# Performance work log

Hardware: AMD Instinct MI355X
Metric: run time of the kernel (lower is better)

The kernel has to match this reference:

```python
import jax, jax.numpy as jnp
import numpy as np

B, S, D = 2, 2048, 1024
H, KS = 16, 64

def setup_inputs() -> dict:
    key = jax.random.key(0)
    k1, k2, k3, k4, k5 = jax.random.split(key, 5)
    return {
        "x": jax.random.normal(k1, (B, S, D), dtype=jnp.float32),
        "Wq": jax.random.normal(k2, (D, KS, H), dtype=jnp.float32) * 0.02,
        "Wk": jax.random.normal(k3, (D, KS, H), dtype=jnp.float32) * 0.02,
        "Wv": jax.random.normal(k4, (D, KS, H), dtype=jnp.float32) * 0.02,
        "kernel": jax.random.normal(k5, (H * KS, KS), dtype=jnp.float32) * 0.02,
    }

def reference(x, Wq, Wk, Wv, kernel):
    b, s, d = x.shape
    ks, h = Wq.shape[1], Wq.shape[2]
    # projections: heads-last layout [b, s, ks, h]
    q = jnp.einsum('bsd,dkh->bskh', x, Wq)
    k = jnp.einsum('bsd,dkh->bskh', x, Wk)
    v = jnp.einsum('bsd,dkh->bskh', x, Wv)
    # scores [b, i(query), l(key), h]
    scores = jnp.einsum('bikh,blkh->bilh', q, k) / jnp.sqrt(jnp.float32(ks))
    # strictly-upper-triangular (future) mask, as in the original:
    # band_part(ones,0,-1) - eye  ->  1 where l > i
    li = jnp.arange(s)
    mask = (li[None, :] > li[:, None]).astype(jnp.float32)  # [s, s]
    scores = scores - 1e8 * mask[None, :, :, None]
    weights = jax.nn.softmax(scores, axis=2)  # softmax over key axis l
    heads = jnp.einsum('bilh,blkh->bikh', weights, v)  # [b, s, ks, h]
    heads = heads.reshape(b, s, ks * h)  # row-major flatten of (ks, h), matching tf.reshape
    return heads @ kernel  # [b, s, ks]
```

## Files before the change

### kernel.cpp

```cpp
#include <hip/hip_runtime.h>
#include <hip/hip_bf16.h>

#define BB 2
#define SS 2048
#define DD 1024
#define HH 16
#define KSZ 64

typedef __attribute__((ext_vector_type(8))) short s16x8;
typedef __attribute__((ext_vector_type(4))) float f32x4;
typedef __attribute__((ext_vector_type(8))) unsigned short u16x8;
typedef __attribute__((ext_vector_type(4))) unsigned short u16x4;
typedef __attribute__((ext_vector_type(2))) unsigned int u32x2;
typedef unsigned short u16;

__device__ __forceinline__ u16 bf16rne(float f) {
  unsigned int u = __float_as_uint(f);
  unsigned int r = (u + 0x7FFFu + ((u >> 16) & 1u)) >> 16;
  return (u16)r;
}

__device__ __forceinline__ void lds_dma16(const u16* g, u16* l) {
  __builtin_amdgcn_global_load_lds(
      (const __attribute__((address_space(1))) unsigned int*)(const void*)g,
      (__attribute__((address_space(3))) unsigned int*)(void*)l, 16, 0, 0);
}

__global__ __launch_bounds__(256) void prep_all(
    const float* __restrict__ x, const float* __restrict__ Wq,
    const float* __restrict__ Wk, const float* __restrict__ Wv,
    const float* __restrict__ kern, u16* __restrict__ xb,
    u16* __restrict__ Wt, u16* __restrict__ BpT) {
  __shared__ float Ts[64][65];
  const int bid = blockIdx.x;
  const int tid = threadIdx.x;
  if (bid < 2048) {
    int idx = (bid * 256 + tid) * 8;
    float4 a = *(const float4*)(x + idx);
    float4 b = *(const float4*)(x + idx + 4);
    u16x8 v;
    v[0] = bf16rne(a.x); v[1] = bf16rne(a.y); v[2] = bf16rne(a.z); v[3] = bf16rne(a.w);
    v[4] = bf16rne(b.x); v[5] = bf16rne(b.y); v[6] = bf16rne(b.z); v[7] = bf16rne(b.w);
    *(u16x8*)(xb + idx) = v;
  } else if (bid < 2816) {
    const int bx = bid - 2048;
    const int p = bx >> 8, rem = bx & 255;
    const int d0 = (rem & 15) * 64, n0 = (rem >> 4) * 64;
    const float* W = (p == 0) ? Wq : (p == 1) ? Wk : Wv;
    u16* Wo = Wt + (size_t)p * DD * DD;
    #pragma unroll
    for (int i = 0; i < 4; ++i) {
      int f4 = tid + i * 256;
      int r = f4 >> 4, c4 = f4 & 15;
      float4 v = *(const float4*)(W + (size_t)(d0 + r) * DD + n0 + c4 * 4);
      Ts[r][c4 * 4 + 0] = v.x; Ts[r][c4 * 4 + 1] = v.y;
      Ts[r][c4 * 4 + 2] = v.z; Ts[r][c4 * 4 + 3] = v.w;
    }
    __syncthreads();
    #pragma unroll
    for (int i = 0; i < 4; ++i) {
      int ch = tid + i * 256;
      int n = ch >> 4, d4 = ch & 15;
      u16x4 o;
      #pragma unroll
      for (int j = 0; j < 4; ++j) o[j] = bf16rne(Ts[d4 * 4 + j][n]);
      *(u16x4*)(Wo + (size_t)(n0 + n) * DD + d0 + d4 * 4) = o;
    }
  } else {
    const int n = bid - 2816;
    const int k4 = tid * 4;
    u16x4 o;
    #pragma unroll
    for (int j = 0; j < 4; ++j) {
      int kp = k4 + j;
      int h = kp >> 6, k = kp & 63;
      o[j] = bf16rne(kern[(size_t)(k * HH + h) * KSZ + n]);
    }
    *(u16x4*)(BpT + (size_t)n * (HH * KSZ) + k4) = o;
  }
}

__global__ __launch_bounds__(256) void proj_kernel(
    const u16* __restrict__ xb, const u16* __restrict__ Wt,
    u16* __restrict__ qkvT) {
  const int xcd = blockIdx.x & 7;
  const int idx = blockIdx.x >> 3;
  const int mt = (xcd >> 1) * 8 + (idx & 7);
  const int nt = (xcd & 1) * 4 + ((idx >> 3) & 3);
  const int p  = idx >> 5;
  const int m0 = mt * 128, n0 = nt * 128;
  const u16* W = Wt + (size_t)p * DD * DD;
  u16* outp = qkvT + (size_t)p * (BB * HH * SS * KSZ);

  __shared__ __align__(16) unsigned char raw[49152];
  u16* lds = (u16*)raw;
  u16* Cs  = (u16*)raw;

  const int tid = threadIdx.x;
  const int wave = tid >> 6, lane = tid & 63;
  const int g = lane >> 4, c = lane & 15;
  const int mbase = (wave & 1) * 64, nbase = (wave >> 1) * 64;

  const int lr = lane >> 2, lc = lane & 3;
  const int swz = (lc ^ ((lr >> 1) & 3)) * 8;
  const int rA0 = (wave * 2 + 0) * 16;
  const int rA1 = (wave * 2 + 1) * 16;
  const u16* srcA0 = xb + (size_t)(m0 + rA0 + lr) * DD + swz;
  const u16* srcA1 = xb + (size_t)(m0 + rA1 + lr) * DD + swz;
  const u16* srcB0 = W  + (size_t)(n0 + rA0 + lr) * DD + swz;
  const u16* srcB1 = W  + (size_t)(n0 + rA1 + lr) * DD + swz;
  const int sl0 = rA0 * 32, sl1 = rA1 * 32;

  f32x4 acc[4][4];
  #pragma unroll
  for (int i = 0; i < 4; ++i)
    #pragma unroll
    for (int j = 0; j < 4; ++j) acc[i][j] = {0.f, 0.f, 0.f, 0.f};

  {
    u16* A0 = lds;                u16* B0 = lds + 4096;
    u16* A1 = lds + 8192;         u16* B1 = lds + 8192 + 4096;
    lds_dma16(srcA0, A0 + sl0);       lds_dma16(srcA1, A0 + sl1);
    lds_dma16(srcB0, B0 + sl0);       lds_dma16(srcB1, B0 + sl1);
    lds_dma16(srcA0 + 32, A1 + sl0);  lds_dma16(srcA1 + 32, A1 + sl1);
    lds_dma16(srcB0 + 32, B1 + sl0);  lds_dma16(srcB1 + 32, B1 + sl1);
  }

  const int jsw = (c >> 1) & 3;
  int cr = 0;
  #pragma unroll 1
  for (int t = 0; t < 31; ++t) {
    asm volatile("s_waitcnt vmcnt(4)" ::: "memory");
    __builtin_amdgcn_s_barrier();
    __builtin_amdgcn_sched_barrier(0);
    if (t <= 29) {
      const int st = cr ? cr - 1 : 2;
      const int ko = (t + 2) * 32;
      u16* An = lds + st * 8192;
      u16* Bn = An + 4096;
      lds_dma16(srcA0 + ko, An + sl0);  lds_dma16(srcA1 + ko, An + sl1);
      lds_dma16(srcB0 + ko, Bn + sl0);  lds_dma16(srcB1 + ko, Bn + sl1);
    }
    u16* Ac = lds + cr * 8192;
    u16* Bc = Ac + 4096;
    s16x8 af[4], bfr[4];
    #pragma unroll
    for (int mf = 0; mf < 4; ++mf)
      af[mf] = *(const s16x8*)&Ac[(mbase + mf * 16 + c) * 32 + ((g ^ jsw) * 8)];
    #pragma unroll
    for (int nf = 0; nf < 4; ++nf)
      bfr[nf] = *(const s16x8*)&Bc[(nbase + nf * 16 + c) * 32 + ((g ^ jsw) * 8)];
    #pragma unroll
    for (int mf = 0; mf < 4; ++mf)
      #pragma unroll
      for (int nf = 0; nf < 4; ++nf)
        acc[mf][nf] = __builtin_amdgcn_mfma_f32_16x16x32_bf16(
            af[mf], bfr[nf], acc[mf][nf], 0, 0, 0);
    cr = (cr >= 2) ? 0 : cr + 1;
  }
  asm volatile("s_waitcnt vmcnt(0)" ::: "memory");
  __builtin_amdgcn_s_barrier();
  __builtin_amdgcn_sched_barrier(0);
  {
    u16* Ac = lds + cr * 8192;
    u16* Bc = Ac + 4096;
    s16x8 af[4], bfr[4];
    #pragma unroll
    for (int mf = 0; mf < 4; ++mf)
      af[mf] = *(const s16x8*)&Ac[(mbase + mf * 16 + c) * 32 + ((g ^ jsw) * 8)];
    #pragma unroll
    for (int nf = 0; nf < 4; ++nf)
      bfr[nf] = *(const s16x8*)&Bc[(nbase + nf * 16 + c) * 32 + ((g ^ jsw) * 8)];
    #pragma unroll
    for (int mf = 0; mf < 4; ++mf)
      #pragma unroll
      for (int nf = 0; nf < 4; ++nf)
        acc[mf][nf] = __builtin_amdgcn_mfma_f32_16x16x32_bf16(
            af[mf], bfr[nf], acc[mf][nf], 0, 0, 0);
  }
  __syncthreads();

  const float cscale = (p == 0) ? 0.125f * 1.44269504f : 1.0f;
  #pragma unroll
  for (int mf = 0; mf < 4; ++mf)
    #pragma unroll
    for (int nf = 0; nf < 4; ++nf)
      #pragma unroll
      for (int r = 0; r < 4; ++r)
        Cs[(mbase + mf * 16 + g * 4 + r) * 136 + nbase + nf * 16 + c] =
            bf16rne(acc[mf][nf][r] * cscale);
  __syncthreads();
  const int b = m0 >> 11;
  if (p < 2) {
    int hh = tid >> 4, si = tid & 15;
    #pragma unroll
    for (int i = 0; i < 8; ++i) {
      int row = i * 16 + si;
      int s = (m0 + row) & 2047;
      u16x8 v;
      #pragma unroll
      for (int kp = 0; kp < 8; ++kp) v[kp] = Cs[row * 136 + kp * 16 + hh];
      *(u16x8*)(outp + ((size_t)(b * HH + hh) * SS + s) * KSZ + (n0 >> 4)) = v;
    }
  } else {
    const int s0 = m0 & 2047;
    #pragma unroll
    for (int i = 0; i < 8; ++i) {
      int chunk = tid + i * 256;
      int colid = chunk >> 4;
      int hh = colid >> 3, kp = colid & 7;
      int s8 = chunk & 15;
      u16x8 v;
      #pragma unroll
      for (int j = 0; j < 8; ++j) v[j] = Cs[(s8 * 8 + j) * 136 + kp * 16 + hh];
      *(u16x8*)(outp + ((size_t)(b * HH + hh) * KSZ + (n0 >> 4) + kp) * SS +
                s0 + s8 * 8) = v;
    }
  }
}

__global__ __launch_bounds__(256) void attn_kernel(
    const u16* __restrict__ qkvT, u16* __restrict__ headsB) {
  const int bid = blockIdx.x;
  const int hb = bid & 31;
  const int u  = bid >> 5;
  const int it = (u & 1) ? (31 - (u >> 1)) : (u >> 1);
  const int h = hb & 15, b = hb >> 4;
  const size_t plane = (size_t)(b * HH + h) * SS * KSZ;
  const size_t PSZ = (size_t)BB * HH * SS * KSZ;
  const u16* Qg = qkvT + plane;
  const u16* Kg = qkvT + PSZ + plane;
  const u16* Vg = qkvT + 2 * PSZ + plane;

  __shared__ u16 Ks[2][64 * 64];
  __shared__ u16 Vt[2][64 * 64];
  __shared__ u16 Ps[64 * 72];

  const int tid = threadIdx.x;
  const int lane = tid & 63;
  const int g = lane >> 4, c = lane & 15;
  const int wq0 = (tid >> 6) * 16;
  const int sr = tid >> 3, sc = tid & 7;
  const int soA = sr * 64 + ((sc ^ (sr & 7)) * 8);
  const int soB = soA + 32 * 64;

  s16x8 bq0 = *(const s16x8*)(Qg + (size_t)(it * 64 + wq0 + c) * KSZ + g * 8);
  s16x8 bq1 = *(const s16x8*)(Qg + (size_t)(it * 64 + wq0 + c) * KSZ + 32 + g * 8);

  u16x8 kr0 = *(const u16x8*)(Kg + (size_t)sr * KSZ + sc * 8);
  u16x8 kr1 = *(const u16x8*)(Kg + (size_t)(sr + 32) * KSZ + sc * 8);
  u16x8 vr0 = *(const u16x8*)(Vg + (size_t)sr * SS + sc * 8);
  u16x8 vr1 = *(const u16x8*)(Vg + (size_t)(sr + 32) * SS + sc * 8);
  *(u16x8*)&Ks[0][soA] = kr0; *(u16x8*)&Ks[0][soB] = kr1;
  *(u16x8*)&Vt[0][soA] = vr0; *(u16x8*)&Vt[0][soB] = vr1;
  if (it >= 1) {
    kr0 = *(const u16x8*)(Kg + (size_t)(64 + sr) * KSZ + sc * 8);
    kr1 = *(const u16x8*)(Kg + (size_t)(64 + sr + 32) * KSZ + sc * 8);
    vr0 = *(const u16x8*)(Vg + (size_t)sr * SS + 64 + sc * 8);
    vr1 = *(const u16x8*)(Vg + (size_t)(sr + 32) * SS + 64 + sc * 8);
  }
  __syncthreads();

  f32x4 o[4];
  #pragma unroll
  for (int mf = 0; mf < 4; ++mf) o[mf] = {0.f, 0.f, 0.f, 0.f};
  float l_i = 0.f;
  const int cswz = c & 7;

  #pragma unroll 1
  for (int t = 0; t <= it; ++t) {
    const int buf = t & 1;
    if (t < it) {
      const int nb = buf ^ 1;
      *(u16x8*)&Ks[nb][soA] = kr0; *(u16x8*)&Ks[nb][soB] = kr1;
      *(u16x8*)&Vt[nb][soA] = vr0; *(u16x8*)&Vt[nb][soB] = vr1;
      if (t + 2 <= it) {
        const int kv2 = t + 2;
        kr0 = *(const u16x8*)(Kg + (size_t)(kv2 * 64 + sr) * KSZ + sc * 8);
        kr1 = *(const u16x8*)(Kg + (size_t)(kv2 * 64 + sr + 32) * KSZ + sc * 8);
        vr0 = *(const u16x8*)(Vg + (size_t)sr * SS + kv2 * 64 + sc * 8);
        vr1 = *(const u16x8*)(Vg + (size_t)(sr + 32) * SS + kv2 * 64 + sc * 8);
      }
    }
    f32x4 s[4];
    #pragma unroll
    for (int mf = 0; mf < 4; ++mf) s[mf] = {0.f, 0.f, 0.f, 0.f};
    #pragma unroll
    for (int ks = 0; ks < 2; ++ks) {
      const s16x8 bq = ks ? bq1 : bq0;
      #pragma unroll
      for (int mf = 0; mf < 4; ++mf) {
        s16x8 ak = *(const s16x8*)&Ks[buf][(mf * 16 + c) * 64 +
                                          (((ks * 4 + g) ^ cswz) * 8)];
        s[mf] = __builtin_amdgcn_mfma_f32_16x16x32_bf16(ak, bq, s[mf], 0, 0, 0);
      }
    }
    if (t == it) {
      const int qloc = wq0 + c;
      #pragma unroll
      for (int mf = 0; mf < 4; ++mf)
        #pragma unroll
        for (int r = 0; r < 4; ++r)
          if (mf * 16 + g * 4 + r > qloc) s[mf][r] = -1e30f;
    }
    float ps = 0.f;
    #pragma unroll
    for (int mf = 0; mf < 4; ++mf) {
      float p0 = __builtin_amdgcn_exp2f(s[mf][0]);
      float p1 = __builtin_amdgcn_exp2f(s[mf][1]);
      float p2 = __builtin_amdgcn_exp2f(s[mf][2]);
      float p3 = __builtin_amdgcn_exp2f(s[mf][3]);
      ps += (p0 + p1) + (p2 + p3);
      u32x2 d;
      d[0] = (__float_as_uint(p0) >> 16) | (__float_as_uint(p1) & 0xFFFF0000u);
      d[1] = (__float_as_uint(p2) >> 16) | (__float_as_uint(p3) & 0xFFFF0000u);
      *(u32x2*)&Ps[(wq0 + c) * 72 + mf * 16 + g * 4] = d;
    }
    l_i += ps;
    #pragma unroll
    for (int ks = 0; ks < 2; ++ks) {
      s16x8 bp = *(const s16x8*)&Ps[(wq0 + c) * 72 + ks * 32 + g * 8];
      #pragma unroll
      for (int mf = 0; mf < 4; ++mf) {
        s16x8 av = *(const s16x8*)&Vt[buf][(mf * 16 + c) * 64 +
                                           (((ks * 4 + g) ^ cswz) * 8)];
        o[mf] = __builtin_amdgcn_mfma_f32_16x16x32_bf16(av, bp, o[mf], 0, 0, 0);
      }
    }
    __syncthreads();
  }
  l_i += __shfl_xor(l_i, 16);
  l_i += __shfl_xor(l_i, 32);
  const float inv = 1.0f / l_i;
  const int q = it * 64 + wq0 + c;
  #pragma unroll
  for (int mf = 0; mf < 4; ++mf) {
    u16x4 hv;
    #pragma unroll
    for (int r = 0; r < 4; ++r) hv[r] = bf16rne(o[mf][r] * inv);
    *(u16x4*)(headsB + plane + (size_t)q * KSZ + mf * 16 + g * 4) = hv;
  }
}

__global__ __launch_bounds__(256) void out_kernel(
    const u16* __restrict__ headsB, const u16* __restrict__ BpT,
    float* __restrict__ out) {
  const int m0 = blockIdx.x * 16;
  const int tid = threadIdx.x;
  const int wave = tid >> 6, lane = tid & 63;
  const int g = lane >> 4, c = lane & 15;

  const int m = m0 + c;
  const int b = m >> 11, s = m & 2047;

  f32x4 acc[4];
  #pragma unroll
  for (int nf = 0; nf < 4; ++nf) acc[nf] = {0.f, 0.f, 0.f, 0.f};

  #pragma unroll
  for (int it = 0; it < 8; ++it) {
    const int kb = wave * 256 + it * 32;
    const int hh = kb >> 6, kk = (kb & 63) + g * 8;
    s16x8 a = *(const s16x8*)(headsB +
        ((size_t)(b * HH + hh) * SS + s) * KSZ + kk);
    #pragma unroll
    for (int nf = 0; nf < 4; ++nf) {
      s16x8 bf = *(const s16x8*)(BpT +
          (size_t)(nf * 16 + c) * (HH * KSZ) + kb + g * 8);
      acc[nf] = __builtin_amdgcn_mfma_f32_16x16x32_bf16(a, bf, acc[nf], 0, 0, 0);
    }
  }

  __shared__ __align__(16) float red[4][64][16];
  #pragma unroll
  for (int nf = 0; nf < 4; ++nf)
    *(f32x4*)&red[wave][lane][nf * 4] = acc[nf];
  __syncthreads();

  const int mi = tid >> 4, n4 = (tid & 15) * 4;
  const int gg = mi >> 2, rr = mi & 3;
  float4 res;
  float* rp = &res.x;
  #pragma unroll
  for (int j = 0; j < 4; ++j) {
    int n = n4 + j;
    int cc = n & 15, nf = n >> 4;
    rp[j] = red[0][gg * 16 + cc][nf * 4 + rr] + red[1][gg * 16 + cc][nf * 4 + rr] +
            red[2][gg * 16 + cc][nf * 4 + rr] + red[3][gg * 16 + cc][nf * 4 + rr];
  }
  *(float4*)(out + (size_t)(m0 + mi) * KSZ + n4) = res;
}

extern "C" void kernel_launch(void* const* d_in, const int* in_sizes, int n_in,
                              void* d_out, int out_size, void* d_ws, size_t ws_size,
                              hipStream_t stream) {
  const float* x    = (const float*)d_in[0];
  const float* Wq   = (const float*)d_in[1];
  const float* Wk   = (const float*)d_in[2];
  const float* Wv   = (const float*)d_in[3];
  const float* kern = (const float*)d_in[4];
  float* out = (float*)d_out;

  u16* xb     = (u16*)d_ws;
  u16* Wt     = xb + (size_t)4096 * 1024;
  u16* qkvT   = Wt + (size_t)3 * 1024 * 1024;
  u16* headsB = qkvT + (size_t)3 * BB * HH * SS * KSZ;
  u16* BpT    = headsB + (size_t)BB * HH * SS * KSZ;

  prep_all<<<dim3(2880), 256, 0, stream>>>(x, Wq, Wk, Wv, kern, xb, Wt, BpT);
  proj_kernel<<<dim3(768), 256, 0, stream>>>(xb, Wt, qkvT);
  attn_kernel<<<dim3(1024), 256, 0, stream>>>(qkvT, headsB);
  out_kernel<<<dim3(256), 256, 0, stream>>>(headsB, BpT, out);
}
```

Measured before the change: 159.6 us.

## Enlarge attention query tile to 128 rows with 512-thread blocks sharing K/V

The attention kernel now handles 128 query rows per block with 8 waves instead of 64 rows with 4 waves, halving the grid. Each K/V tile staged in shared memory is reused by twice as many queries, which roughly halves global K/V traffic and LDS fill work per query. The causal mask now covers the last two key tiles, so the lower 64 query rows compute one fully masked tile, adding some wasted work. Fewer, larger blocks may also reduce occupancy and worsen load balance across the causal triangle.

```diff
diff --git a/kernel.cpp b/kernel.cpp
--- a/kernel.cpp
+++ b/kernel.cpp
@@ -219,12 +219,12 @@
   }
 }
 
-__global__ __launch_bounds__(256) void attn_kernel(
+__global__ __launch_bounds__(512) void attn_kernel(
     const u16* __restrict__ qkvT, u16* __restrict__ headsB) {
   const int bid = blockIdx.x;
   const int hb = bid & 31;
   const int u  = bid >> 5;
-  const int it = (u & 1) ? (31 - (u >> 1)) : (u >> 1);
+  const int qt = (u & 1) ? (15 - (u >> 1)) : (u >> 1);
   const int h = hb & 15, b = hb >> 4;
   const size_t plane = (size_t)(b * HH + h) * SS * KSZ;
   const size_t PSZ = (size_t)BB * HH * SS * KSZ;
@@ -234,31 +234,26 @@
 
   __shared__ u16 Ks[2][64 * 64];
   __shared__ u16 Vt[2][64 * 64];
-  __shared__ u16 Ps[64 * 72];
+  __shared__ u16 Ps[128 * 72];
 
   const int tid = threadIdx.x;
   const int lane = tid & 63;
   const int g = lane >> 4, c = lane & 15;
   const int wq0 = (tid >> 6) * 16;
   const int sr = tid >> 3, sc = tid & 7;
-  const int soA = sr * 64 + ((sc ^ (sr & 7)) * 8);
-  const int soB = soA + 32 * 64;
-
-  s16x8 bq0 = *(const s16x8*)(Qg + (size_t)(it * 64 + wq0 + c) * KSZ + g * 8);
-  s16x8 bq1 = *(const s16x8*)(Qg + (size_t)(it * 64 + wq0 + c) * KSZ + 32 + g * 8);
-
-  u16x8 kr0 = *(const u16x8*)(Kg + (size_t)sr * KSZ + sc * 8);
-  u16x8 kr1 = *(const u16x8*)(Kg + (size_t)(sr + 32) * KSZ + sc * 8);
-  u16x8 vr0 = *(const u16x8*)(Vg + (size_t)sr * SS + sc * 8);
-  u16x8 vr1 = *(const u16x8*)(Vg + (size_t)(sr + 32) * SS + sc * 8);
-  *(u16x8*)&Ks[0][soA] = kr0; *(u16x8*)&Ks[0][soB] = kr1;
-  *(u16x8*)&Vt[0][soA] = vr0; *(u16x8*)&Vt[0][soB] = vr1;
-  if (it >= 1) {
-    kr0 = *(const u16x8*)(Kg + (size_t)(64 + sr) * KSZ + sc * 8);
-    kr1 = *(const u16x8*)(Kg + (size_t)(64 + sr + 32) * KSZ + sc * 8);
-    vr0 = *(const u16x8*)(Vg + (size_t)sr * SS + 64 + sc * 8);
-    vr1 = *(const u16x8*)(Vg + (size_t)(sr + 32) * SS + 64 + sc * 8);
-  }
+  const int so = sr * 64 + ((sc ^ (sr & 7)) * 8);
+
+  const int nt = 2 * qt + 2;
+
+  s16x8 bq0 = *(const s16x8*)(Qg + (size_t)(qt * 128 + wq0 + c) * KSZ + g * 8);
+  s16x8 bq1 = *(const s16x8*)(Qg + (size_t)(qt * 128 + wq0 + c) * KSZ + 32 + g * 8);
+
+  u16x8 kr = *(const u16x8*)(Kg + (size_t)sr * KSZ + sc * 8);
+  u16x8 vr = *(const u16x8*)(Vg + (size_t)sr * SS + sc * 8);
+  *(u16x8*)&Ks[0][so] = kr;
+  *(u16x8*)&Vt[0][so] = vr;
+  kr = *(const u16x8*)(Kg + (size_t)(64 + sr) * KSZ + sc * 8);
+  vr = *(const u16x8*)(Vg + (size_t)sr * SS + 64 + sc * 8);
   __syncthreads();
 
   f32x4 o[4];
@@ -266,20 +261,18 @@
   for (int mf = 0; mf < 4; ++mf) o[mf] = {0.f, 0.f, 0.f, 0.f};
   float l_i = 0.f;
   const int cswz = c & 7;
+  const int qloc = wq0 + c;
 
   #pragma unroll 1
-  for (int t = 0; t <= it; ++t) {
+  for (int t = 0; t < nt; ++t) {
     const int buf = t & 1;
-    if (t < it) {
+    if (t + 1 < nt) {
       const int nb = buf ^ 1;
-      *(u16x8*)&Ks[nb][soA] = kr0; *(u16x8*)&Ks[nb][soB] = kr1;
-      *(u16x8*)&Vt[nb][soA] = vr0; *(u16x8*)&Vt[nb][soB] = vr1;
-      if (t + 2 <= it) {
-        const int kv2 = t + 2;
-        kr0 = *(const u16x8*)(Kg + (size_t)(kv2 * 64 + sr) * KSZ + sc * 8);
-        kr1 = *(const u16x8*)(Kg + (size_t)(kv2 * 64 + sr + 32) * KSZ + sc * 8);
-        vr0 = *(const u16x8*)(Vg + (size_t)sr * SS + kv2 * 64 + sc * 8);
-        vr1 = *(const u16x8*)(Vg + (size_t)(sr + 32) * SS + kv2 * 64 + sc * 8);
+      *(u16x8*)&Ks[nb][so] = kr;
+      *(u16x8*)&Vt[nb][so] = vr;
+      if (t + 2 < nt) {
+        kr = *(const u16x8*)(Kg + (size_t)((t + 2) * 64 + sr) * KSZ + sc * 8);
+        vr = *(const u16x8*)(Vg + (size_t)sr * SS + (t + 2) * 64 + sc * 8);
       }
     }
     f32x4 s[4];
@@ -295,13 +288,13 @@
         s[mf] = __builtin_amdgcn_mfma_f32_16x16x32_bf16(ak, bq, s[mf], 0, 0, 0);
       }
     }
-    if (t == it) {
-      const int qloc = wq0 + c;
+    if (t >= 2 * qt) {
+      const int rel = (t - 2 * qt) * 64;
       #pragma unroll
       for (int mf = 0; mf < 4; ++mf)
         #pragma unroll
         for (int r = 0; r < 4; ++r)
-          if (mf * 16 + g * 4 + r > qloc) s[mf][r] = -1e30f;
+          if (rel + mf * 16 + g * 4 + r > qloc) s[mf][r] = -1e30f;
     }
     float ps = 0.f;
     #pragma unroll
@@ -314,12 +307,12 @@
       u32x2 d;
       d[0] = (__float_as_uint(p0) >> 16) | (__float_as_uint(p1) & 0xFFFF0000u);
       d[1] = (__float_as_uint(p2) >> 16) | (__float_as_uint(p3) & 0xFFFF0000u);
-      *(u32x2*)&Ps[(wq0 + c) * 72 + mf * 16 + g * 4] = d;
+      *(u32x2*)&Ps[qloc * 72 + mf * 16 + g * 4] = d;
     }
     l_i += ps;
     #pragma unroll
     for (int ks = 0; ks < 2; ++ks) {
-      s16x8 bp = *(const s16x8*)&Ps[(wq0 + c) * 72 + ks * 32 + g * 8];
+      s16x8 bp = *(const s16x8*)&Ps[qloc * 72 + ks * 32 + g * 8];
       #pragma unroll
       for (int mf = 0; mf < 4; ++mf) {
         s16x8 av = *(const s16x8*)&Vt[buf][(mf * 16 + c) * 64 +
@@ -332,7 +325,7 @@
   l_i += __shfl_xor(l_i, 16);
   l_i += __shfl_xor(l_i, 32);
   const float inv = 1.0f / l_i;
-  const int q = it * 64 + wq0 + c;
+  const int q = qt * 128 + wq0 + c;
   #pragma unroll
   for (int mf = 0; mf < 4; ++mf) {
     u16x4 hv;
@@ -409,6 +402,6 @@
 
   prep_all<<<dim3(2880), 256, 0, stream>>>(x, Wq, Wk, Wv, kern, xb, Wt, BpT);
   proj_kernel<<<dim3(768), 256, 0, stream>>>(xb, Wt, qkvT);
-  attn_kernel<<<dim3(1024), 256, 0, stream>>>(qkvT, headsB);
+  attn_kernel<<<dim3(512), 512, 0, stream>>>(qkvT, headsB);
   out_kernel<<<dim3(256), 256, 0, stream>>>(headsB, BpT, out);
 }
```

Result: slower. 165.2 us (+3.5%).

## Double query tile per attention block to reuse K/V loads across 128 queries

Applied to the files above, without the earlier changes.

The attention kernel now handles 128 query rows per block instead of 64, with each wave owning two 16-row sub-tiles that share every K and V LDS fragment read. Grid size halves to 512 blocks and the causal tile schedule is remapped to pair short and long query tiles. This cuts global and LDS traffic for K/V per query and doubles MFMA work per LDS read. In exchange it raises register pressure, uses more LDS for Ps, and gives fewer, longer blocks, which can hurt occupancy and load balance.

```diff
diff --git a/kernel.cpp b/kernel.cpp
--- a/kernel.cpp
+++ b/kernel.cpp
@@ -223,8 +223,8 @@
     const u16* __restrict__ qkvT, u16* __restrict__ headsB) {
   const int bid = blockIdx.x;
   const int hb = bid & 31;
-  const int u  = bid >> 5;
-  const int it = (u & 1) ? (31 - (u >> 1)) : (u >> 1);
+  const int q5 = bid >> 5;
+  const int qt = (q5 < 8) ? q5 : 23 - q5;
   const int h = hb & 15, b = hb >> 4;
   const size_t plane = (size_t)(b * HH + h) * SS * KSZ;
   const size_t PSZ = (size_t)BB * HH * SS * KSZ;
@@ -234,18 +234,25 @@
 
   __shared__ u16 Ks[2][64 * 64];
   __shared__ u16 Vt[2][64 * 64];
-  __shared__ u16 Ps[64 * 72];
+  __shared__ u16 Ps[128 * 72];
 
   const int tid = threadIdx.x;
-  const int lane = tid & 63;
+  const int wave = tid >> 6, lane = tid & 63;
   const int g = lane >> 4, c = lane & 15;
-  const int wq0 = (tid >> 6) * 16;
+  const int wq0 = wave * 32;
   const int sr = tid >> 3, sc = tid & 7;
   const int soA = sr * 64 + ((sc ^ (sr & 7)) * 8);
   const int soB = soA + 32 * 64;
 
-  s16x8 bq0 = *(const s16x8*)(Qg + (size_t)(it * 64 + wq0 + c) * KSZ + g * 8);
-  s16x8 bq1 = *(const s16x8*)(Qg + (size_t)(it * 64 + wq0 + c) * KSZ + 32 + g * 8);
+  const int nt = 2 * qt + 2;
+
+  s16x8 bq[2][2];
+  #pragma unroll
+  for (int sq = 0; sq < 2; ++sq) {
+    const size_t qrow = (size_t)(qt * 128 + wq0 + sq * 16 + c) * KSZ;
+    bq[sq][0] = *(const s16x8*)(Qg + qrow + g * 8);
+    bq[sq][1] = *(const s16x8*)(Qg + qrow + 32 + g * 8);
+  }
 
   u16x8 kr0 = *(const u16x8*)(Kg + (size_t)sr * KSZ + sc * 8);
   u16x8 kr1 = *(const u16x8*)(Kg + (size_t)(sr + 32) * KSZ + sc * 8);
@@ -253,28 +260,28 @@
   u16x8 vr1 = *(const u16x8*)(Vg + (size_t)(sr + 32) * SS + sc * 8);
   *(u16x8*)&Ks[0][soA] = kr0; *(u16x8*)&Ks[0][soB] = kr1;
   *(u16x8*)&Vt[0][soA] = vr0; *(u16x8*)&Vt[0][soB] = vr1;
-  if (it >= 1) {
-    kr0 = *(const u16x8*)(Kg + (size_t)(64 + sr) * KSZ + sc * 8);
-    kr1 = *(const u16x8*)(Kg + (size_t)(64 + sr + 32) * KSZ + sc * 8);
-    vr0 = *(const u16x8*)(Vg + (size_t)sr * SS + 64 + sc * 8);
-    vr1 = *(const u16x8*)(Vg + (size_t)(sr + 32) * SS + 64 + sc * 8);
-  }
+  kr0 = *(const u16x8*)(Kg + (size_t)(64 + sr) * KSZ + sc * 8);
+  kr1 = *(const u16x8*)(Kg + (size_t)(64 + sr + 32) * KSZ + sc * 8);
+  vr0 = *(const u16x8*)(Vg + (size_t)sr * SS + 64 + sc * 8);
+  vr1 = *(const u16x8*)(Vg + (size_t)(sr + 32) * SS + 64 + sc * 8);
   __syncthreads();
 
-  f32x4 o[4];
-  #pragma unroll
-  for (int mf = 0; mf < 4; ++mf) o[mf] = {0.f, 0.f, 0.f, 0.f};
-  float l_i = 0.f;
+  f32x4 o[2][4];
+  #pragma unroll
+  for (int sq = 0; sq < 2; ++sq)
+    #pragma unroll
+    for (int mf = 0; mf < 4; ++mf) o[sq][mf] = {0.f, 0.f, 0.f, 0.f};
+  float l_i[2] = {0.f, 0.f};
   const int cswz = c & 7;
 
   #pragma unroll 1
-  for (int t = 0; t <= it; ++t) {
+  for (int t = 0; t < nt; ++t) {
     const int buf = t & 1;
-    if (t < it) {
+    if (t + 1 < nt) {
       const int nb = buf ^ 1;
       *(u16x8*)&Ks[nb][soA] = kr0; *(u16x8*)&Ks[nb][soB] = kr1;
       *(u16x8*)&Vt[nb][soA] = vr0; *(u16x8*)&Vt[nb][soB] = vr1;
-      if (t + 2 <= it) {
+      if (t + 2 < nt) {
         const int kv2 = t + 2;
         kr0 = *(const u16x8*)(Kg + (size_t)(kv2 * 64 + sr) * KSZ + sc * 8);
         kr1 = *(const u16x8*)(Kg + (size_t)(kv2 * 64 + sr + 32) * KSZ + sc * 8);
@@ -282,63 +289,83 @@
         vr1 = *(const u16x8*)(Vg + (size_t)(sr + 32) * SS + kv2 * 64 + sc * 8);
       }
     }
-    f32x4 s[4];
-    #pragma unroll
-    for (int mf = 0; mf < 4; ++mf) s[mf] = {0.f, 0.f, 0.f, 0.f};
+    f32x4 s[2][4];
+    #pragma unroll
+    for (int sq = 0; sq < 2; ++sq)
+      #pragma unroll
+      for (int mf = 0; mf < 4; ++mf) s[sq][mf] = {0.f, 0.f, 0.f, 0.f};
     #pragma unroll
     for (int ks = 0; ks < 2; ++ks) {
-      const s16x8 bq = ks ? bq1 : bq0;
       #pragma unroll
       for (int mf = 0; mf < 4; ++mf) {
         s16x8 ak = *(const s16x8*)&Ks[buf][(mf * 16 + c) * 64 +
                                           (((ks * 4 + g) ^ cswz) * 8)];
-        s[mf] = __builtin_amdgcn_mfma_f32_16x16x32_bf16(ak, bq, s[mf], 0, 0, 0);
+        s[0][mf] = __builtin_amdgcn_mfma_f32_16x16x32_bf16(ak, bq[0][ks],
+                                                           s[0][mf], 0, 0, 0);
+        s[1][mf] = __builtin_amdgcn_mfma_f32_16x16x32_bf16(ak, bq[1][ks],
+                                                           s[1][mf], 0, 0, 0);
       }
     }
-    if (t == it) {
-      const int qloc = wq0 + c;
-      #pragma unroll
-      for (int mf = 0; mf < 4; ++mf)
+    if (t >= 2 * qt) {
+      const int rel = (t - 2 * qt) * 64;
+      #pragma unroll
+      for (int sq = 0; sq < 2; ++sq) {
+        const int qloc = wq0 + sq * 16 + c;
         #pragma unroll
-        for (int r = 0; r < 4; ++r)
-          if (mf * 16 + g * 4 + r > qloc) s[mf][r] = -1e30f;
-    }
-    float ps = 0.f;
-    #pragma unroll
-    for (int mf = 0; mf < 4; ++mf) {
-      float p0 = __builtin_amdgcn_exp2f(s[mf][0]);
-      float p1 = __builtin_amdgcn_exp2f(s[mf][1]);
-      float p2 = __builtin_amdgcn_exp2f(s[mf][2]);
-      float p3 = __builtin_amdgcn_exp2f(s[mf][3]);
-      ps += (p0 + p1) + (p2 + p3);
-      u32x2 d;
-      d[0] = (__float_as_uint(p0) >> 16) | (__float_as_uint(p1) & 0xFFFF0000u);
-      d[1] = (__float_as_uint(p2) >> 16) | (__float_as_uint(p3) & 0xFFFF0000u);
-      *(u32x2*)&Ps[(wq0 + c) * 72 + mf * 16 + g * 4] = d;
-    }
-    l_i += ps;
+        for (int mf = 0; mf < 4; ++mf)
+          #pragma unroll
+          for (int r = 0; r < 4; ++r)
+            if (rel + mf * 16 + g * 4 + r > qloc) s[sq][mf][r] = -1e30f;
+      }
+    }
+    #pragma unroll
+    for (int sq = 0; sq < 2; ++sq) {
+      float ps = 0.f;
+      const int qloc = wq0 + sq * 16 + c;
+      #pragma unroll
+      for (int mf = 0; mf < 4; ++mf) {
+        float p0 = __builtin_amdgcn_exp2f(s[sq][mf][0]);
+        float p1 = __builtin_amdgcn_exp2f(s[sq][mf][1]);
+        float p2 = __builtin_amdgcn_exp2f(s[sq][mf][2]);
+        float p3 = __builtin_amdgcn_exp2f(s[sq][mf][3]);
+        ps += (p0 + p1) + (p2 + p3);
+        u32x2 d;
+        d[0] = (__float_as_uint(p0) >> 16) | (__float_as_uint(p1) & 0xFFFF0000u);
+        d[1] = (__float_as_uint(p2) >> 16) | (__float_as_uint(p3) & 0xFFFF0000u);
+        *(u32x2*)&Ps[qloc * 72 + mf * 16 + g * 4] = d;
+      }
+      l_i[sq] += ps;
+    }
     #pragma unroll
     for (int ks = 0; ks < 2; ++ks) {
-      s16x8 bp = *(const s16x8*)&Ps[(wq0 + c) * 72 + ks * 32 + g * 8];
+      s16x8 bp0 = *(const s16x8*)&Ps[(wq0 + c) * 72 + ks * 32 + g * 8];
+      s16x8 bp1 = *(const s16x8*)&Ps[(wq0 + 16 + c) * 72 + ks * 32 + g * 8];
       #pragma unroll
       for (int mf = 0; mf < 4; ++mf) {
         s16x8 av = *(const s16x8*)&Vt[buf][(mf * 16 + c) * 64 +
                                            (((ks * 4 + g) ^ cswz) * 8)];
-        o[mf] = __builtin_amdgcn_mfma_f32_16x16x32_bf16(av, bp, o[mf], 0, 0, 0);
+        o[0][mf] = __builtin_amdgcn_mfma_f32_16x16x32_bf16(av, bp0, o[0][mf],
+                                                           0, 0, 0);
+        o[1][mf] = __builtin_amdgcn_mfma_f32_16x16x32_bf16(av, bp1, o[1][mf],
+                                                           0, 0, 0);
       }
     }
     __syncthreads();
   }
-  l_i += __shfl_xor(l_i, 16);
-  l_i += __shfl_xor(l_i, 32);
-  const float inv = 1.0f / l_i;
-  const int q = it * 64 + wq0 + c;
-  #pragma unroll
-  for (int mf = 0; mf < 4; ++mf) {
-    u16x4 hv;
-    #pragma unroll
-    for (int r = 0; r < 4; ++r) hv[r] = bf16rne(o[mf][r] * inv);
-    *(u16x4*)(headsB + plane + (size_t)q * KSZ + mf * 16 + g * 4) = hv;
+  #pragma unroll
+  for (int sq = 0; sq < 2; ++sq) {
+    float l = l_i[sq];
+    l += __shfl_xor(l, 16);
+    l += __shfl_xor(l, 32);
+    const float inv = 1.0f / l;
+    const int q = qt * 128 + wq0 + sq * 16 + c;
+    #pragma unroll
+    for (int mf = 0; mf < 4; ++mf) {
+      u16x4 hv;
+      #pragma unroll
+      for (int r = 0; r < 4; ++r) hv[r] = bf16rne(o[sq][mf][r] * inv);
+      *(u16x4*)(headsB + plane + (size_t)q * KSZ + mf * 16 + g * 4) = hv;
+    }
   }
 }
 
@@ -409,6 +436,6 @@
 
   prep_all<<<dim3(2880), 256, 0, stream>>>(x, Wq, Wk, Wv, kern, xb, Wt, BpT);
   proj_kernel<<<dim3(768), 256, 0, stream>>>(xb, Wt, qkvT);
-  attn_kernel<<<dim3(1024), 256, 0, stream>>>(qkvT, headsB);
+  attn_kernel<<<dim3(512), 256, 0, stream>>>(qkvT, headsB);
   out_kernel<<<dim3(256), 256, 0, stream>>>(headsB, BpT, out);
 }
```

Measured after the change: 165.8 us. +3.9%, slower.

## Keep softmax probabilities in registers and feed PV via 16x16x16 MFMA

Applied to the files above, without the earlier changes.

Removes the LDS round-trip for the probability tile. The exp results are packed to bf16 with v_cvt_pk_bf16_f32 and used directly as the B operand of 16x16x16 MFMAs, whose K layout matches the score accumulator layout. It also adds s_setprio around the MFMA blocks, an occupancy hint of 4 blocks, a different causal-tile ordering for load balance, and rounding instead of truncation for P. The cost is twice as many MFMA instructions at half the K depth, and smaller LDS reads for V.

```diff
diff --git a/kernel.cpp b/kernel.cpp
--- a/kernel.cpp
+++ b/kernel.cpp
@@ -8,6 +8,7 @@
 #define KSZ 64
 
 typedef __attribute__((ext_vector_type(8))) short s16x8;
+typedef __attribute__((ext_vector_type(4))) short s16x4;
 typedef __attribute__((ext_vector_type(4))) float f32x4;
 typedef __attribute__((ext_vector_type(8))) unsigned short u16x8;
 typedef __attribute__((ext_vector_type(4))) unsigned short u16x4;
@@ -19,6 +20,28 @@
   unsigned int r = (u + 0x7FFFu + ((u >> 16) & 1u)) >> 16;
   return (u16)r;
 }
+
+__device__ __forceinline__ unsigned int cvtpk_bf16(float lo, float hi) {
+  unsigned int r;
+  asm("v_cvt_pk_bf16_f32 %0, %1, %2" : "=v"(r) : "v"(lo), "v"(hi));
+  return r;
+}
+
+#if __has_builtin(__builtin_amdgcn_mfma_f32_16x16x16_bf16)
+__device__ __forceinline__ f32x4 mfma16(s16x4 a, s16x4 b, f32x4 c) {
+  return __builtin_amdgcn_mfma_f32_16x16x16_bf16(a, b, c, 0, 0, 0);
+}
+#elif __has_builtin(__builtin_amdgcn_mfma_f32_16x16x16bf16_1k)
+__device__ __forceinline__ f32x4 mfma16(s16x4 a, s16x4 b, f32x4 c) {
+  return __builtin_amdgcn_mfma_f32_16x16x16bf16_1k(a, b, c, 0, 0, 0);
+}
+#else
+__device__ __forceinline__ f32x4 mfma16(s16x4 a, s16x4 b, f32x4 c) {
+  asm("s_nop 1\n\tv_mfma_f32_16x16x16_bf16 %0, %1, %2, %0"
+      : "+v"(c) : "v"(a), "v"(b));
+  return c;
+}
+#endif
 
 __device__ __forceinline__ void lds_dma16(const u16* g, u16* l) {
   __builtin_amdgcn_global_load_lds(
@@ -219,12 +242,13 @@
   }
 }
 
-__global__ __launch_bounds__(256) void attn_kernel(
+__global__ __launch_bounds__(256, 4) void attn_kernel(
     const u16* __restrict__ qkvT, u16* __restrict__ headsB) {
   const int bid = blockIdx.x;
   const int hb = bid & 31;
   const int u  = bid >> 5;
-  const int it = (u & 1) ? (31 - (u >> 1)) : (u >> 1);
+  const int x  = u & 7, w = u >> 3;
+  const int it = (w == 0) ? x : (w == 1) ? 15 - x : (w == 2) ? 16 + x : 31 - x;
   const int h = hb & 15, b = hb >> 4;
   const size_t plane = (size_t)(b * HH + h) * SS * KSZ;
   const size_t PSZ = (size_t)BB * HH * SS * KSZ;
@@ -234,7 +258,6 @@
 
   __shared__ u16 Ks[2][64 * 64];
   __shared__ u16 Vt[2][64 * 64];
-  __shared__ u16 Ps[64 * 72];
 
   const int tid = threadIdx.x;
   const int lane = tid & 63;
@@ -253,12 +276,10 @@
   u16x8 vr1 = *(const u16x8*)(Vg + (size_t)(sr + 32) * SS + sc * 8);
   *(u16x8*)&Ks[0][soA] = kr0; *(u16x8*)&Ks[0][soB] = kr1;
   *(u16x8*)&Vt[0][soA] = vr0; *(u16x8*)&Vt[0][soB] = vr1;
-  if (it >= 1) {
-    kr0 = *(const u16x8*)(Kg + (size_t)(64 + sr) * KSZ + sc * 8);
-    kr1 = *(const u16x8*)(Kg + (size_t)(64 + sr + 32) * KSZ + sc * 8);
-    vr0 = *(const u16x8*)(Vg + (size_t)sr * SS + 64 + sc * 8);
-    vr1 = *(const u16x8*)(Vg + (size_t)(sr + 32) * SS + 64 + sc * 8);
-  }
+  kr0 = *(const u16x8*)(Kg + (size_t)(64 + sr) * KSZ + sc * 8);
+  kr1 = *(const u16x8*)(Kg + (size_t)(64 + sr + 32) * KSZ + sc * 8);
+  vr0 = *(const u16x8*)(Vg + (size_t)sr * SS + 64 + sc * 8);
+  vr1 = *(const u16x8*)(Vg + (size_t)(sr + 32) * SS + 64 + sc * 8);
   __syncthreads();
 
   f32x4 o[4];
@@ -266,6 +287,7 @@
   for (int mf = 0; mf < 4; ++mf) o[mf] = {0.f, 0.f, 0.f, 0.f};
   float l_i = 0.f;
   const int cswz = c & 7;
+  const int qloc = wq0 + c;
 
   #pragma unroll 1
   for (int t = 0; t <= it; ++t) {
@@ -285,6 +307,7 @@
     f32x4 s[4];
     #pragma unroll
     for (int mf = 0; mf < 4; ++mf) s[mf] = {0.f, 0.f, 0.f, 0.f};
+    __builtin_amdgcn_s_setprio(1);
     #pragma unroll
     for (int ks = 0; ks < 2; ++ks) {
       const s16x8 bq = ks ? bq1 : bq0;
@@ -295,38 +318,39 @@
         s[mf] = __builtin_amdgcn_mfma_f32_16x16x32_bf16(ak, bq, s[mf], 0, 0, 0);
       }
     }
+    __builtin_amdgcn_s_setprio(0);
     if (t == it) {
-      const int qloc = wq0 + c;
       #pragma unroll
       for (int mf = 0; mf < 4; ++mf)
         #pragma unroll
         for (int r = 0; r < 4; ++r)
           if (mf * 16 + g * 4 + r > qloc) s[mf][r] = -1e30f;
     }
-    float ps = 0.f;
+    s16x4 bp[4];
     #pragma unroll
     for (int mf = 0; mf < 4; ++mf) {
       float p0 = __builtin_amdgcn_exp2f(s[mf][0]);
       float p1 = __builtin_amdgcn_exp2f(s[mf][1]);
       float p2 = __builtin_amdgcn_exp2f(s[mf][2]);
       float p3 = __builtin_amdgcn_exp2f(s[mf][3]);
-      ps += (p0 + p1) + (p2 + p3);
-      u32x2 d;
-      d[0] = (__float_as_uint(p0) >> 16) | (__float_as_uint(p1) & 0xFFFF0000u);
-      d[1] = (__float_as_uint(p2) >> 16) | (__float_as_uint(p3) & 0xFFFF0000u);
-      *(u32x2*)&Ps[(wq0 + c) * 72 + mf * 16 + g * 4] = d;
-    }
-    l_i += ps;
-    #pragma unroll
-    for (int ks = 0; ks < 2; ++ks) {
-      s16x8 bp = *(const s16x8*)&Ps[(wq0 + c) * 72 + ks * 32 + g * 8];
-      #pragma unroll
-      for (int mf = 0; mf < 4; ++mf) {
-        s16x8 av = *(const s16x8*)&Vt[buf][(mf * 16 + c) * 64 +
-                                           (((ks * 4 + g) ^ cswz) * 8)];
-        o[mf] = __builtin_amdgcn_mfma_f32_16x16x32_bf16(av, bp, o[mf], 0, 0, 0);
+      l_i += (p0 + p1) + (p2 + p3);
+      u32x2 pk;
+      pk[0] = cvtpk_bf16(p0, p1);
+      pk[1] = cvtpk_bf16(p2, p3);
+      bp[mf] = __builtin_bit_cast(s16x4, pk);
+    }
+    __builtin_amdgcn_s_setprio(1);
+    #pragma unroll
+    for (int mf = 0; mf < 4; ++mf) {
+      #pragma unroll
+      for (int kb = 0; kb < 4; ++kb) {
+        s16x4 av = *(const s16x4*)&Vt[buf][(mf * 16 + c) * 64 +
+                                           (((kb * 2 + (g >> 1)) ^ cswz) * 8) +
+                                           (g & 1) * 4];
+        o[mf] = mfma16(av, bp[kb], o[mf]);
       }
     }
+    __builtin_amdgcn_s_setprio(0);
     __syncthreads();
   }
   l_i += __shfl_xor(l_i, 16);
```

New measurement: 158.3 us. Within noise of the previous version (-0.8%).
